# Performance work log

Measured on AMD Instinct MI355X. Metric: run time of the kernel, lower is better.

## Reference

```python
import jax, jax.numpy as jnp
import numpy as np

NLOC = 10  # local nodes per element (cubic DG triangle)


def setup_inputs() -> dict:
    key = jax.random.key(0)
    ks = jax.random.split(key, 6)
    nele, nloc, ngi = 500000, NLOC, 13
    return {
        "r0": jax.random.normal(ks[0], (nele * nloc,), dtype=jnp.float32),
        "c_i": jax.random.normal(ks[1], (nele * nloc,), dtype=jnp.float32),
        "c_n": jax.random.normal(ks[2], (nele, 1, nloc), dtype=jnp.float32),
        "k": jnp.ones((1,), dtype=jnp.float32),
        "dt": jnp.ones((1,), dtype=jnp.float32),
        "n": jax.random.normal(ks[3], (nloc, ngi), dtype=jnp.float32),
        "nx": jax.random.normal(ks[4], (nele, 2, nloc, ngi), dtype=jnp.float32),
        "detwei": jax.random.uniform(ks[5], (nele, ngi), dtype=jnp.float32),
    }


def reference(r0, c_i, c_n, k, dt, n, nx, detwei):
    nele, _, nloc, ngi = nx.shape
    c_i = c_i.reshape(nele, 1, nloc)               # [e,1,l]
    # stiffness: sum over spatial dims of grad-grad quadrature contraction
    nx1nx1 = jnp.einsum('eig,ejg,eg->eij', nx[:, 0], nx[:, 0], detwei)
    nx2nx2 = jnp.einsum('eig,ejg,eg->eij', nx[:, 1], nx[:, 1], detwei)
    nxnx = (nx1nx1 + nx2nx2) * k                   # [e,i,j] * [1]
    # mass matrix per element (shared shape funcs, per-element detwei)
    nn = jnp.einsum('ig,jg,eg->eij', n, n, detwei)
    # transient branch (config.isTransient = True)
    nn_dt = nn / dt
    nxnx = nn_dt + nxnx
    r0 = r0.reshape(nele, nloc, 1)
    r0 = r0 + jnp.matmul(nn_dt, jnp.swapaxes(c_n, 1, 2))   # [e,i,1]
    r0 = r0.reshape(-1)
    r0 = r0 - jnp.matmul(nxnx, jnp.swapaxes(c_i, 1, 2)).reshape(-1)
    diagA = jnp.diagonal(nxnx, axis1=-2, axis2=-1)          # [e,nloc]
    bdiagA = nxnx
    return (bdiagA, diagA, r0)
```

## Files before the change

### kernel.cpp

```cpp
#include <hip/hip_runtime.h>

#define NLOC  10
#define NGI   13
#define NPAIR 55
#define EPB   16
#define TPB   64

#define W_DW   4160
#define W_N    4368
#define W_TOT  4498

#define GE_NX  1040
#define GE_DW  1092
#define NITER  18

typedef float vf2 __attribute__((ext_vector_type(2)));

__device__ __forceinline__ constexpr int pidx(int i, int j) {
    return i * NLOC - (i * (i - 1)) / 2 + (j - i);
}

__device__ __forceinline__ void stage16(const float* gsrc, float* lds) {
    __builtin_amdgcn_global_load_lds(
        (const __attribute__((address_space(1))) void*)gsrc,
        (__attribute__((address_space(3))) void*)lds, 16, 0, 0);
}

__global__ __launch_bounds__(TPB) void fem_kernel(
    const float* __restrict__ r0g,
    const float* __restrict__ cig,
    const float* __restrict__ cng,
    const float* __restrict__ kp,
    const float* __restrict__ dtp,
    const float* __restrict__ nmat,
    const float* __restrict__ nx,
    const float* __restrict__ dwei,
    float* __restrict__ out,
    int nele)
{
    __shared__ float sm[W_TOT];

    const int  t   = threadIdx.x;
    const long e0  = (long)blockIdx.x * EPB;
    const int  rem = min(EPB, nele - (int)e0);

    for (int w = t; w < 130; w += TPB) sm[W_N + w] = nmat[w];

    const float* nxsrc = nx   + (size_t)e0 * 260;
    const float* dwsrc = dwei + (size_t)e0 * 13;
    const int capnx = rem * 260;
    const int capdw = rem * 13;
    #pragma unroll
    for (int k = 0; k < 16; ++k) {
        const int G = k * TPB + t;
        if (G * 4 < capnx) stage16(nxsrc + (size_t)G * 4, sm + k * TPB * 4);
    }
    #pragma unroll
    for (int k = 16; k < NITER; ++k) {
        const int G = k * TPB + t;
        if (G < GE_NX) {
            if (G * 4 < capnx) stage16(nxsrc + (size_t)G * 4, sm + k * TPB * 4);
        } else if (G < GE_DW) {
            const int rel = G - GE_NX;
            if (rel * 4 < capdw) stage16(dwsrc + (size_t)rel * 4, sm + k * TPB * 4);
        }
    }

    const int  eloc = t >> 2;
    const int  d    = (t >> 1) & 1;
    const int  h    = t & 1;
    const int  q    = t & 3;
    const long e    = e0 + eloc;
    const bool live = eloc < rem;
    const long ee   = live ? e : (long)(nele - 1);

    const float kk  = kp[0];
    const float idt = 1.0f / dtp[0];

    float civ[NLOC], dif[NLOC];
    {
        const vf2* ci2 = reinterpret_cast<const vf2*>(cig + (size_t)ee * 10);
        const vf2* cn2 = reinterpret_cast<const vf2*>(cng + (size_t)ee * 10);
        #pragma unroll
        for (int u2 = 0; u2 < 5; ++u2) {
            vf2 a = ci2[u2], b = cn2[u2];
            civ[2*u2]   = a.x; civ[2*u2+1] = a.y;
            dif[2*u2]   = b.x - a.x; dif[2*u2+1] = b.y - a.y;
        }
    }

    asm volatile("s_waitcnt vmcnt(0)" ::: "memory");

    const float* smnx = sm + eloc * 260 + d * 130;
    const float* smdw = sm + W_DW + eloc * 13;
    const float* smn  = sm + W_N;

    float acc[NPAIR];
    #pragma unroll
    for (int p = 0; p < NPAIR; ++p) acc[p] = 0.0f;
    float r0a[NLOC];
    #pragma unroll
    for (int i = 0; i < NLOC; ++i) r0a[i] = 0.0f;

    #pragma unroll
    for (int it = 0; it < 7; ++it) {
        const int   graw = 2 * it + h;
        const int   g    = graw < NGI ? graw : NGI - 1;
        const float wv   = graw < NGI ? kk * smdw[g] : 0.0f;
        float col[NLOC];
        #pragma unroll
        for (int l = 0; l < NLOC; ++l) col[l] = smnx[l * 13 + g];
        float u = 0.0f;
        #pragma unroll
        for (int l = 0; l < NLOC; ++l) u = fmaf(col[l], civ[l], u);
        const float uw = u * wv;
        #pragma unroll
        for (int i = 0; i < NLOC; ++i) {
            const float ti = col[i] * wv;
            #pragma unroll
            for (int j = i; j < NLOC; ++j)
                acc[pidx(i, j)] = fmaf(ti, col[j], acc[pidx(i, j)]);
            r0a[i] = fmaf(-col[i], uw, r0a[i]);
        }
    }

    #pragma unroll
    for (int it = 0; it < 4; ++it) {
        const int   graw = q + 4 * it;
        const int   g    = graw < NGI ? graw : NGI - 1;
        const float wv   = graw < NGI ? idt * smdw[g] : 0.0f;
        float ncol[NLOC];
        #pragma unroll
        for (int l = 0; l < NLOC; ++l) ncol[l] = smn[l * 13 + g];
        float wd = 0.0f;
        #pragma unroll
        for (int l = 0; l < NLOC; ++l) wd = fmaf(ncol[l], dif[l], wd);
        #pragma unroll
        for (int i = 0; i < NLOC; ++i) {
            const float ti = ncol[i] * wv;
            #pragma unroll
            for (int j = i; j < NLOC; ++j)
                acc[pidx(i, j)] = fmaf(ti, ncol[j], acc[pidx(i, j)]);
            r0a[i] = fmaf(ti, wd, r0a[i]);
        }
    }

    #pragma unroll
    for (int p = 0; p < NPAIR; ++p) {
        acc[p] += __shfl_xor(acc[p], 1);
        acc[p] += __shfl_xor(acc[p], 2);
    }
    #pragma unroll
    for (int i = 0; i < NLOC; ++i) {
        r0a[i] += __shfl_xor(r0a[i], 1);
        r0a[i] += __shfl_xor(r0a[i], 2);
    }

    if (live) {
        float* obd = out + (size_t)e * 100;
        float* odg = out + (size_t)nele * 100 + (size_t)e * 10;
        float* oro = out + (size_t)nele * 110 + (size_t)e * 10;
        const float* r0s = r0g + (size_t)e * 10;
        #pragma unroll
        for (int i = 0; i < NLOC; ++i) {
            if ((i & 3) == q) {
                float row[NLOC];
                #pragma unroll
                for (int j = 0; j < NLOC; ++j) {
                    const int lo = i < j ? i : j, hi = i < j ? j : i;
                    row[j] = acc[pidx(lo, hi)];
                }
                #pragma unroll
                for (int u2 = 0; u2 < 5; ++u2) {
                    vf2 v = { row[2*u2], row[2*u2+1] };
                    *reinterpret_cast<vf2*>(obd + i * 10 + 2 * u2) = v;
                }
                odg[i] = row[i];
                oro[i] = r0s[i] + r0a[i];
            }
        }
    }
}

extern "C" void kernel_launch(void* const* d_in, const int* in_sizes, int n_in,
                              void* d_out, int out_size, void* d_ws, size_t ws_size,
                              hipStream_t stream) {
    const float* r0   = (const float*)d_in[0];
    const float* ci   = (const float*)d_in[1];
    const float* cn   = (const float*)d_in[2];
    const float* k    = (const float*)d_in[3];
    const float* dt   = (const float*)d_in[4];
    const float* nmat = (const float*)d_in[5];
    const float* nx   = (const float*)d_in[6];
    const float* dw   = (const float*)d_in[7];
    const int nele = in_sizes[7] / NGI;

    const int nb = (nele + EPB - 1) / EPB;
    fem_kernel<<<nb, TPB, 0, stream>>>(r0, ci, cn, k, dt, nmat, nx, dw,
                                       (float*)d_out, nele);
}
```

Measured before the change: 221.8 us.

## Stage nx in two halves to halve LDS footprint and raise occupancy

```diff
diff --git a/kernel.cpp b/kernel.cpp
--- a/kernel.cpp
+++ b/kernel.cpp
@@ -6,13 +6,9 @@
 #define EPB   16
 #define TPB   64
 
-#define W_DW   4160
-#define W_N    4368
-#define W_TOT  4498
-
-#define GE_NX  1040
-#define GE_DW  1092
-#define NITER  18
+#define W_DW   2112
+#define W_N    2320
+#define W_TOT  2450
 
 typedef float vf2 __attribute__((ext_vector_type(2)));
 
@@ -26,7 +22,7 @@
         (__attribute__((address_space(3))) void*)lds, 16, 0, 0);
 }
 
-__global__ __launch_bounds__(TPB) void fem_kernel(
+__global__ __launch_bounds__(TPB, 4) void fem_kernel(
     const float* __restrict__ r0g,
     const float* __restrict__ cig,
     const float* __restrict__ cng,
@@ -44,31 +40,7 @@
     const long e0  = (long)blockIdx.x * EPB;
     const int  rem = min(EPB, nele - (int)e0);
 
-    for (int w = t; w < 130; w += TPB) sm[W_N + w] = nmat[w];
-
-    const float* nxsrc = nx   + (size_t)e0 * 260;
-    const float* dwsrc = dwei + (size_t)e0 * 13;
-    const int capnx = rem * 260;
-    const int capdw = rem * 13;
-    #pragma unroll
-    for (int k = 0; k < 16; ++k) {
-        const int G = k * TPB + t;
-        if (G * 4 < capnx) stage16(nxsrc + (size_t)G * 4, sm + k * TPB * 4);
-    }
-    #pragma unroll
-    for (int k = 16; k < NITER; ++k) {
-        const int G = k * TPB + t;
-        if (G < GE_NX) {
-            if (G * 4 < capnx) stage16(nxsrc + (size_t)G * 4, sm + k * TPB * 4);
-        } else if (G < GE_DW) {
-            const int rel = G - GE_NX;
-            if (rel * 4 < capdw) stage16(dwsrc + (size_t)rel * 4, sm + k * TPB * 4);
-        }
-    }
-
     const int  eloc = t >> 2;
-    const int  d    = (t >> 1) & 1;
-    const int  h    = t & 1;
     const int  q    = t & 3;
     const long e    = e0 + eloc;
     const bool live = eloc < rem;
@@ -77,6 +49,8 @@
     const float kk  = kp[0];
     const float idt = 1.0f / dtp[0];
 
+    for (int w = t; w < 130; w += TPB) sm[W_N + w] = nmat[w];
+
     float civ[NLOC], dif[NLOC];
     {
         const vf2* ci2 = reinterpret_cast<const vf2*>(cig + (size_t)ee * 10);
@@ -89,11 +63,24 @@
         }
     }
 
+    #pragma unroll
+    for (int k2 = 0; k2 < 10; ++k2) {
+        const int G = k2 * TPB + t;
+        if (G < 528) {
+            const int u = G / 33, r = G - u * 33;
+            if (e0 + u < nele)
+                stage16(nx + ((size_t)(e0 + u) * 260 + r * 4), sm + k2 * 256);
+        } else if (G < 580) {
+            const int rel = (G - 528) * 4;
+            if (rel + 4 <= rem * 13)
+                stage16(dwei + (size_t)e0 * 13 + rel, sm + k2 * 256);
+        }
+    }
     asm volatile("s_waitcnt vmcnt(0)" ::: "memory");
 
-    const float* smnx = sm + eloc * 260 + d * 130;
+    const float* smn  = sm + W_N;
     const float* smdw = sm + W_DW + eloc * 13;
-    const float* smn  = sm + W_N;
+    const float* smx0 = sm + eloc * 132;
 
     float acc[NPAIR];
     #pragma unroll
@@ -103,13 +90,13 @@
     for (int i = 0; i < NLOC; ++i) r0a[i] = 0.0f;
 
     #pragma unroll
-    for (int it = 0; it < 7; ++it) {
-        const int   graw = 2 * it + h;
+    for (int it = 0; it < 4; ++it) {
+        const int   graw = q + 4 * it;
         const int   g    = graw < NGI ? graw : NGI - 1;
         const float wv   = graw < NGI ? kk * smdw[g] : 0.0f;
         float col[NLOC];
         #pragma unroll
-        for (int l = 0; l < NLOC; ++l) col[l] = smnx[l * 13 + g];
+        for (int l = 0; l < NLOC; ++l) col[l] = smx0[l * 13 + g];
         float u = 0.0f;
         #pragma unroll
         for (int l = 0; l < NLOC; ++l) u = fmaf(col[l], civ[l], u);
@@ -123,7 +110,6 @@
             r0a[i] = fmaf(-col[i], uw, r0a[i]);
         }
     }
-
     #pragma unroll
     for (int it = 0; it < 4; ++it) {
         const int   graw = q + 4 * it;
@@ -142,6 +128,44 @@
             for (int j = i; j < NLOC; ++j)
                 acc[pidx(i, j)] = fmaf(ti, ncol[j], acc[pidx(i, j)]);
             r0a[i] = fmaf(ti, wd, r0a[i]);
+        }
+    }
+
+    asm volatile("s_waitcnt lgkmcnt(0)" ::: "memory");
+    __builtin_amdgcn_sched_barrier(0);
+
+    #pragma unroll
+    for (int k2 = 0; k2 < 9; ++k2) {
+        const int G = k2 * TPB + t;
+        if (G < 528) {
+            const int u = G / 33, r = G - u * 33;
+            if (e0 + u < nele)
+                stage16(nx + ((size_t)(e0 + u) * 260 + 128 + r * 4), sm + k2 * 256);
+        }
+    }
+    asm volatile("s_waitcnt vmcnt(0)" ::: "memory");
+
+    const float* smx1 = sm + eloc * 132 + 2;
+
+    #pragma unroll
+    for (int it = 0; it < 4; ++it) {
+        const int   graw = q + 4 * it;
+        const int   g    = graw < NGI ? graw : NGI - 1;
+        const float wv   = graw < NGI ? kk * smdw[g] : 0.0f;
+        float col[NLOC];
+        #pragma unroll
+        for (int l = 0; l < NLOC; ++l) col[l] = smx1[l * 13 + g];
+        float u = 0.0f;
+        #pragma unroll
+        for (int l = 0; l < NLOC; ++l) u = fmaf(col[l], civ[l], u);
+        const float uw = u * wv;
+        #pragma unroll
+        for (int i = 0; i < NLOC; ++i) {
+            const float ti = col[i] * wv;
+            #pragma unroll
+            for (int j = i; j < NLOC; ++j)
+                acc[pidx(i, j)] = fmaf(ti, col[j], acc[pidx(i, j)]);
+            r0a[i] = fmaf(-col[i], uw, r0a[i]);
         }
     }
 
```

Result: slower. 546.1 us (+146.2%).
